# Optimization experiments

Measured on AMD Instinct MI355X. Metric: run time of the kernel, lower is better.

Reference implementation:

```python
import jax, jax.numpy as jnp
import numpy as np

D_MODEL = 512
HIDDEN_MULT = 4
D_FF = D_MODEL * HIDDEN_MULT
B, L = 4, 1024


def setup_inputs() -> dict:
    key = jax.random.key(0)
    ks = jax.random.split(key, 7)
    s1 = 1.0 / np.sqrt(D_MODEL)
    s2 = 1.0 / np.sqrt(D_FF)
    return {
        "x": jax.random.normal(ks[0], (B, L, D_MODEL), dtype=jnp.float32),
        "W1": jax.random.uniform(ks[1], (D_FF, D_MODEL), minval=-s1, maxval=s1, dtype=jnp.float32),
        "b1": jax.random.uniform(ks[2], (D_FF,), minval=-s1, maxval=s1, dtype=jnp.float32),
        "W2": jax.random.uniform(ks[3], (D_MODEL, D_FF), minval=-s2, maxval=s2, dtype=jnp.float32),
        "b2": jax.random.uniform(ks[4], (D_MODEL,), minval=-s2, maxval=s2, dtype=jnp.float32),
        "Lambda_raw_F": jax.random.uniform(ks[5], (D_FF, D_MODEL), minval=-3.0, maxval=3.0, dtype=jnp.float32),
        "Gamma_F": jax.random.uniform(ks[6], (D_FF, D_MODEL), minval=-0.5 * s1, maxval=0.5 * s1, dtype=jnp.float32),
    }


def _stp_forward(x, W1, b1, W2, b2, Lambda_raw_F, Gamma_F):
    # x: (B, L, D)
    retention = 1.0 - jax.nn.sigmoid(Lambda_raw_F)  # (d_ff, D)
    gamma = Gamma_F
    # static contribution of W1: (B, L, d_ff)
    static_h = jnp.einsum('bld,fd->blf', x, W1) + b1

    def step(F_state, inputs):
        # F_state: (B, d_ff, D); x_t: (B, D); sh_t: (B, d_ff)
        x_t, sh_t = inputs
        h_pre = sh_t + jnp.einsum('bfd,bd->bf', F_state, x_t)
        h = jax.nn.gelu(h_pre, approximate=False)
        out = jnp.einsum('bf,df->bd', h, W2) + b2
        # Hebbian outer-product update
        F_new = retention[None] * F_state + gamma[None] * (h_pre[:, :, None] * x_t[:, None, :])
        return F_new, out

    F0 = jnp.zeros((x.shape[0], W1.shape[0], W1.shape[1]), dtype=x.dtype)
    xs = (jnp.swapaxes(x, 0, 1), jnp.swapaxes(static_h, 0, 1))  # (L, B, ...)
    _, ys = jax.lax.scan(step, F0, xs)
    return jnp.swapaxes(ys, 0, 1)  # (B, L, D)


def reference(x, W1, b1, W2, b2, Lambda_raw_F, Gamma_F):
    return _stp_forward(x, W1, b1, W2, b2, Lambda_raw_F, Gamma_F)
```

## Files before the change

### kernel.cpp

```cpp
#include <hip/hip_runtime.h>
#include <cstdint>

#define DM   512
#define DFF  2048
#define BSZ  4
#define LSEQ 1024

__device__ __forceinline__ float4 f4fma(float4 a, float4 b, float4 c) {
    return make_float4(fmaf(a.x, b.x, c.x), fmaf(a.y, b.y, c.y),
                       fmaf(a.z, b.z, c.z), fmaf(a.w, b.w, c.w));
}
__device__ __forceinline__ float4 f4mul(float4 a, float4 b) {
    return make_float4(a.x * b.x, a.y * b.y, a.z * b.z, a.w * b.w);
}
__device__ __forceinline__ float4 f4fmas(float4 a, float s, float4 c) {
    return make_float4(fmaf(a.x, s, c.x), fmaf(a.y, s, c.y),
                       fmaf(a.z, s, c.z), fmaf(a.w, s, c.w));
}

__device__ __forceinline__ float red32(float p) {
    int t;
    t = __builtin_amdgcn_update_dpp(0, __float_as_int(p), 0xB1, 0xF, 0xF, true);
    p += __int_as_float(t);
    t = __builtin_amdgcn_update_dpp(0, __float_as_int(p), 0x4E, 0xF, 0xF, true);
    p += __int_as_float(t);
    p += __int_as_float(__builtin_amdgcn_ds_swizzle(__float_as_int(p), 0x101F));
    p += __int_as_float(__builtin_amdgcn_ds_swizzle(__float_as_int(p), 0x201F));
    p += __int_as_float(__builtin_amdgcn_ds_swizzle(__float_as_int(p), 0x401F));
    return p;
}

__global__ __launch_bounds__(256, 4)
void stp_scan(const float* __restrict__ x,
              const float* __restrict__ Lam,
              const float* __restrict__ Gam,
              float* __restrict__ hbuf)
{
    const int lane = threadIdx.x & 63;
    const int wid  = threadIdx.x >> 6;
    const int j    = lane & 31;
    const int h    = lane >> 5;
    const int b    = blockIdx.x >> 8;
    const int f    = ((blockIdx.x & 255) << 3) + (wid << 1) + h;

    const float4* __restrict__ x4 =
        reinterpret_cast<const float4*>(x + (size_t)b * LSEQ * DM);
    float* __restrict__ hrow = hbuf + (size_t)b * LSEQ * DFF + f;

    float4 F0 = make_float4(0.f,0.f,0.f,0.f), F1 = F0, F2 = F0, F3 = F0;
    float4 R0, R1, R2, R3, G0, G1, G2, G3;
    {
        const float4* lr = reinterpret_cast<const float4*>(Lam + (size_t)f * DM);
        const float4* gr = reinterpret_cast<const float4*>(Gam + (size_t)f * DM);
        float4 l0 = lr[j], l1 = lr[j + 32], l2 = lr[j + 64], l3 = lr[j + 96];
        #define SIGM(dst, src)                                   \
            dst.x = 1.0f / (1.0f + expf(src.x));                 \
            dst.y = 1.0f / (1.0f + expf(src.y));                 \
            dst.z = 1.0f / (1.0f + expf(src.z));                 \
            dst.w = 1.0f / (1.0f + expf(src.w));
        SIGM(R0, l0) SIGM(R1, l1) SIGM(R2, l2) SIGM(R3, l3)
        #undef SIGM
        G0 = gr[j]; G1 = gr[j + 32]; G2 = gr[j + 64]; G3 = gr[j + 96];
    }

#define STP_STEP(T, Xa, Xb, Xc, Xd, SH)                                   \
    {                                                                     \
        float4 a = f4fma(F1, (Xb), f4mul(F0, (Xa)));                      \
        float4 c = f4fma(F3, (Xd), f4mul(F2, (Xc)));                      \
        a.x += c.x; a.y += c.y; a.z += c.z; a.w += c.w;                   \
        float p = (a.x + a.y) + (a.z + a.w);                              \
        p = red32(p);                                                     \
        const float hp = p + (SH);                                        \
        if (j == 0) hrow[(size_t)(T) * DFF] = hp;                         \
        float4 t0 = f4mul(R0, F0), g0 = f4mul(G0, (Xa));                  \
        float4 t1 = f4mul(R1, F1), g1 = f4mul(G1, (Xb));                  \
        float4 t2 = f4mul(R2, F2), g2 = f4mul(G2, (Xc));                  \
        float4 t3 = f4mul(R3, F3), g3 = f4mul(G3, (Xd));                  \
        F0 = f4fmas(g0, hp, t0);                                          \
        F1 = f4fmas(g1, hp, t1);                                          \
        F2 = f4fmas(g2, hp, t2);                                          \
        F3 = f4fmas(g3, hp, t3);                                          \
    }

    float4 xA0 = x4[j], xA1 = x4[j + 32], xA2 = x4[j + 64], xA3 = x4[j + 96];
    float  shA = hrow[0];

    #pragma unroll 1
    for (int t = 0; t < LSEQ; t += 2) {
        const int o1 = (t + 1) * 128;
        float4 xB0 = x4[o1 + j],      xB1 = x4[o1 + 32 + j];
        float4 xB2 = x4[o1 + 64 + j], xB3 = x4[o1 + 96 + j];
        float  shB = hrow[(size_t)(t + 1) * DFF];

        STP_STEP(t, xA0, xA1, xA2, xA3, shA)

        const int t2 = (t + 2 < LSEQ) ? (t + 2) : (LSEQ - 1);
        const int o2 = t2 * 128;
        xA0 = x4[o2 + j];      xA1 = x4[o2 + 32 + j];
        xA2 = x4[o2 + 64 + j]; xA3 = x4[o2 + 96 + j];
        shA = hrow[(size_t)t2 * DFF];

        STP_STEP(t + 1, xB0, xB1, xB2, xB3, shB)
    }
#undef STP_STEP
}

__global__ __launch_bounds__(256)
void gelu_inplace(float4* __restrict__ p, int n4)
{
    int i = blockIdx.x * blockDim.x + threadIdx.x;
    const int stride = gridDim.x * blockDim.x;
    for (; i < n4; i += stride) {
        float4 v = p[i];
        v.x = 0.5f * v.x * (1.0f + erff(v.x * 0.70710678118654752f));
        v.y = 0.5f * v.y * (1.0f + erff(v.y * 0.70710678118654752f));
        v.z = 0.5f * v.z * (1.0f + erff(v.z * 0.70710678118654752f));
        v.w = 0.5f * v.w * (1.0f + erff(v.w * 0.70710678118654752f));
        p[i] = v;
    }
}

__global__ __launch_bounds__(256)
void gemm_nt_bias(const float* __restrict__ A,
                  const float* __restrict__ Bm,
                  const float* __restrict__ bias,
                  float* __restrict__ C,
                  int M, int N, int K)
{
    __shared__ float As[16][68];
    __shared__ float Bs[16][68];

    const int tid = threadIdx.x;
    const int tx  = tid & 15;
    const int ty  = tid >> 4;
    const int row0 = blockIdx.y * 64;
    const int col0 = blockIdx.x * 64;

    const int lr = tid >> 2;
    const int lk = (tid & 3) << 2;

    const float* Aptr = A  + (size_t)(row0 + lr) * K + lk;
    const float* Bptr = Bm + (size_t)(col0 + lr) * K + lk;

    float acc[4][4] = {};
    float4 av = *reinterpret_cast<const float4*>(Aptr);
    float4 bv = *reinterpret_cast<const float4*>(Bptr);

    const int NT = K >> 4;
    for (int kt = 0; kt < NT; ++kt) {
        __syncthreads();
        As[lk + 0][lr] = av.x; As[lk + 1][lr] = av.y;
        As[lk + 2][lr] = av.z; As[lk + 3][lr] = av.w;
        Bs[lk + 0][lr] = bv.x; Bs[lk + 1][lr] = bv.y;
        Bs[lk + 2][lr] = bv.z; Bs[lk + 3][lr] = bv.w;
        __syncthreads();

        if (kt + 1 < NT) {
            av = *reinterpret_cast<const float4*>(Aptr + (kt + 1) * 16);
            bv = *reinterpret_cast<const float4*>(Bptr + (kt + 1) * 16);
        }

        #pragma unroll
        for (int k = 0; k < 16; ++k) {
            float4 a = *reinterpret_cast<const float4*>(&As[k][ty * 4]);
            float4 bb = *reinterpret_cast<const float4*>(&Bs[k][tx * 4]);
            acc[0][0] = fmaf(a.x, bb.x, acc[0][0]);
            acc[0][1] = fmaf(a.x, bb.y, acc[0][1]);
            acc[0][2] = fmaf(a.x, bb.z, acc[0][2]);
            acc[0][3] = fmaf(a.x, bb.w, acc[0][3]);
            acc[1][0] = fmaf(a.y, bb.x, acc[1][0]);
            acc[1][1] = fmaf(a.y, bb.y, acc[1][1]);
            acc[1][2] = fmaf(a.y, bb.z, acc[1][2]);
            acc[1][3] = fmaf(a.y, bb.w, acc[1][3]);
            acc[2][0] = fmaf(a.z, bb.x, acc[2][0]);
            acc[2][1] = fmaf(a.z, bb.y, acc[2][1]);
            acc[2][2] = fmaf(a.z, bb.z, acc[2][2]);
            acc[2][3] = fmaf(a.z, bb.w, acc[2][3]);
            acc[3][0] = fmaf(a.w, bb.x, acc[3][0]);
            acc[3][1] = fmaf(a.w, bb.y, acc[3][1]);
            acc[3][2] = fmaf(a.w, bb.z, acc[3][2]);
            acc[3][3] = fmaf(a.w, bb.w, acc[3][3]);
        }
    }

    const float4 bb = *reinterpret_cast<const float4*>(&bias[col0 + tx * 4]);
    #pragma unroll
    for (int i = 0; i < 4; ++i) {
        float4 o;
        o.x = acc[i][0] + bb.x;
        o.y = acc[i][1] + bb.y;
        o.z = acc[i][2] + bb.z;
        o.w = acc[i][3] + bb.w;
        *reinterpret_cast<float4*>(&C[(size_t)(row0 + ty * 4 + i) * N + col0 + tx * 4]) = o;
    }
}

extern "C" void kernel_launch(void* const* d_in, const int* in_sizes, int n_in,
                              void* d_out, int out_size, void* d_ws, size_t ws_size,
                              hipStream_t stream)
{
    const float* x   = (const float*)d_in[0];
    const float* W1  = (const float*)d_in[1];
    const float* b1  = (const float*)d_in[2];
    const float* W2  = (const float*)d_in[3];
    const float* b2  = (const float*)d_in[4];
    const float* Lam = (const float*)d_in[5];
    const float* Gam = (const float*)d_in[6];
    float* out  = (float*)d_out;
    float* hbuf = (float*)d_ws;

    const int M = BSZ * LSEQ;

    gemm_nt_bias<<<dim3(DFF / 64, M / 64), dim3(256), 0, stream>>>(
        x, W1, b1, hbuf, M, DFF, DM);

    stp_scan<<<dim3(BSZ * (DFF / 8)), dim3(256), 0, stream>>>(x, Lam, Gam, hbuf);

    gelu_inplace<<<dim3(2048), dim3(256), 0, stream>>>(
        reinterpret_cast<float4*>(hbuf), M * DFF / 4);

    gemm_nt_bias<<<dim3(DM / 64, M / 64), dim3(256), 0, stream>>>(
        hbuf, W2, b2, out, M, DM, DFF);
}
```

Baseline: 836.4 us.

## Stage x timesteps through double-buffered LDS and use packed FP32 math

Each block now loads the x row for a timestep once into a double-buffered shared-memory tile and synchronizes between steps, instead of every wave re-reading x from global memory. The inner products and state update are rewritten with v_pk_mul/v_pk_fma packed FP32 inline asm, and the cross-lane reduction uses row_shr DPP plus a broadcast swizzle. This cuts global load traffic and VALU instruction count, but adds two __syncthreads per step pair that couple the four waves, and inline asm may limit compiler scheduling.

After: 777.9 us. 1.08x faster.

```diff
diff --git a/kernel.cpp b/kernel.cpp
--- a/kernel.cpp
+++ b/kernel.cpp
@@ -6,29 +6,27 @@
 #define BSZ  4
 #define LSEQ 1024
 
-__device__ __forceinline__ float4 f4fma(float4 a, float4 b, float4 c) {
-    return make_float4(fmaf(a.x, b.x, c.x), fmaf(a.y, b.y, c.y),
-                       fmaf(a.z, b.z, c.z), fmaf(a.w, b.w, c.w));
-}
-__device__ __forceinline__ float4 f4mul(float4 a, float4 b) {
-    return make_float4(a.x * b.x, a.y * b.y, a.z * b.z, a.w * b.w);
-}
-__device__ __forceinline__ float4 f4fmas(float4 a, float s, float4 c) {
-    return make_float4(fmaf(a.x, s, c.x), fmaf(a.y, s, c.y),
-                       fmaf(a.z, s, c.z), fmaf(a.w, s, c.w));
-}
-
-__device__ __forceinline__ float red32(float p) {
-    int t;
-    t = __builtin_amdgcn_update_dpp(0, __float_as_int(p), 0xB1, 0xF, 0xF, true);
-    p += __int_as_float(t);
-    t = __builtin_amdgcn_update_dpp(0, __float_as_int(p), 0x4E, 0xF, 0xF, true);
-    p += __int_as_float(t);
-    p += __int_as_float(__builtin_amdgcn_ds_swizzle(__float_as_int(p), 0x101F));
-    p += __int_as_float(__builtin_amdgcn_ds_swizzle(__float_as_int(p), 0x201F));
-    p += __int_as_float(__builtin_amdgcn_ds_swizzle(__float_as_int(p), 0x401F));
-    return p;
-}
+typedef __attribute__((ext_vector_type(2))) float f32x2;
+
+__device__ __forceinline__ f32x2 pk_mul(f32x2 a, f32x2 b) {
+    f32x2 d;
+    asm("v_pk_mul_f32 %0, %1, %2" : "=v"(d) : "v"(a), "v"(b));
+    return d;
+}
+__device__ __forceinline__ f32x2 pk_fma(f32x2 a, f32x2 b, f32x2 c) {
+    f32x2 d;
+    asm("v_pk_fma_f32 %0, %1, %2, %3" : "=v"(d) : "v"(a), "v"(b), "v"(c));
+    return d;
+}
+__device__ __forceinline__ f32x2 pk_add(f32x2 a, f32x2 b) {
+    f32x2 d;
+    asm("v_pk_add_f32 %0, %1, %2" : "=v"(d) : "v"(a), "v"(b));
+    return d;
+}
+
+#define DPP_ADD(p, ctrl)                                                     \
+    p += __int_as_float(__builtin_amdgcn_update_dpp(                         \
+        0, __float_as_int(p), (ctrl), 0xF, 0xF, true))
 
 __global__ __launch_bounds__(256, 4)
 void stp_scan(const float* __restrict__ x,
@@ -36,71 +34,104 @@
               const float* __restrict__ Gam,
               float* __restrict__ hbuf)
 {
-    const int lane = threadIdx.x & 63;
-    const int wid  = threadIdx.x >> 6;
+    const int tid  = threadIdx.x;
+    const int lane = tid & 63;
+    const int wid  = tid >> 6;
     const int j    = lane & 31;
     const int h    = lane >> 5;
     const int b    = blockIdx.x >> 8;
     const int f    = ((blockIdx.x & 255) << 3) + (wid << 1) + h;
 
-    const float4* __restrict__ x4 =
+    __shared__ float4 xs[2][128];
+
+    const float4* __restrict__ x4g =
         reinterpret_cast<const float4*>(x + (size_t)b * LSEQ * DM);
-    float* __restrict__ hrow = hbuf + (size_t)b * LSEQ * DFF + f;
-
-    float4 F0 = make_float4(0.f,0.f,0.f,0.f), F1 = F0, F2 = F0, F3 = F0;
-    float4 R0, R1, R2, R3, G0, G1, G2, G3;
+    float* __restrict__ hbase = hbuf + (size_t)b * LSEQ * DFF;
+
+    f32x2 F[8], R[8], G[8];
     {
         const float4* lr = reinterpret_cast<const float4*>(Lam + (size_t)f * DM);
         const float4* gr = reinterpret_cast<const float4*>(Gam + (size_t)f * DM);
-        float4 l0 = lr[j], l1 = lr[j + 32], l2 = lr[j + 64], l3 = lr[j + 96];
-        #define SIGM(dst, src)                                   \
-            dst.x = 1.0f / (1.0f + expf(src.x));                 \
-            dst.y = 1.0f / (1.0f + expf(src.y));                 \
-            dst.z = 1.0f / (1.0f + expf(src.z));                 \
-            dst.w = 1.0f / (1.0f + expf(src.w));
-        SIGM(R0, l0) SIGM(R1, l1) SIGM(R2, l2) SIGM(R3, l3)
-        #undef SIGM
-        G0 = gr[j]; G1 = gr[j + 32]; G2 = gr[j + 64]; G3 = gr[j + 96];
-    }
-
-#define STP_STEP(T, Xa, Xb, Xc, Xd, SH)                                   \
-    {                                                                     \
-        float4 a = f4fma(F1, (Xb), f4mul(F0, (Xa)));                      \
-        float4 c = f4fma(F3, (Xd), f4mul(F2, (Xc)));                      \
-        a.x += c.x; a.y += c.y; a.z += c.z; a.w += c.w;                   \
-        float p = (a.x + a.y) + (a.z + a.w);                              \
-        p = red32(p);                                                     \
-        const float hp = p + (SH);                                        \
-        if (j == 0) hrow[(size_t)(T) * DFF] = hp;                         \
-        float4 t0 = f4mul(R0, F0), g0 = f4mul(G0, (Xa));                  \
-        float4 t1 = f4mul(R1, F1), g1 = f4mul(G1, (Xb));                  \
-        float4 t2 = f4mul(R2, F2), g2 = f4mul(G2, (Xc));                  \
-        float4 t3 = f4mul(R3, F3), g3 = f4mul(G3, (Xd));                  \
-        F0 = f4fmas(g0, hp, t0);                                          \
-        F1 = f4fmas(g1, hp, t1);                                          \
-        F2 = f4fmas(g2, hp, t2);                                          \
-        F3 = f4fmas(g3, hp, t3);                                          \
-    }
-
-    float4 xA0 = x4[j], xA1 = x4[j + 32], xA2 = x4[j + 64], xA3 = x4[j + 96];
-    float  shA = hrow[0];
+        #pragma unroll
+        for (int k = 0; k < 4; ++k) {
+            float4 lv = lr[j + 32 * k];
+            float4 gv = gr[j + 32 * k];
+            f32x2 r0, r1;
+            r0.x = 1.0f / (1.0f + expf(lv.x));
+            r0.y = 1.0f / (1.0f + expf(lv.y));
+            r1.x = 1.0f / (1.0f + expf(lv.z));
+            r1.y = 1.0f / (1.0f + expf(lv.w));
+            R[2 * k] = r0;   R[2 * k + 1] = r1;
+            f32x2 g0; g0.x = gv.x; g0.y = gv.y;
+            f32x2 g1; g1.x = gv.z; g1.y = gv.w;
+            G[2 * k] = g0;   G[2 * k + 1] = g1;
+            f32x2 z; z.x = 0.f; z.y = 0.f;
+            F[2 * k] = z;    F[2 * k + 1] = z;
+        }
+    }
+
+#define STP_STEP(T, CUR, SHV)                                                 \
+    {                                                                         \
+        float4 q0 = xs[CUR][j];                                               \
+        float4 q1 = xs[CUR][j + 32];                                          \
+        float4 q2 = xs[CUR][j + 64];                                          \
+        float4 q3 = xs[CUR][j + 96];                                          \
+        f32x2 x0 = *(f32x2*)&q0.x, x1 = *(f32x2*)&q0.z;                       \
+        f32x2 x2 = *(f32x2*)&q1.x, x3 = *(f32x2*)&q1.z;                       \
+        f32x2 x4_ = *(f32x2*)&q2.x, x5 = *(f32x2*)&q2.z;                      \
+        f32x2 x6 = *(f32x2*)&q3.x, x7 = *(f32x2*)&q3.z;                       \
+        f32x2 a0 = pk_mul(F[0], x0); f32x2 a1 = pk_mul(F[2], x2);             \
+        a0 = pk_fma(F[1], x1, a0);   a1 = pk_fma(F[3], x3, a1);               \
+        a0 = pk_fma(F[4], x4_, a0);  a1 = pk_fma(F[5], x5, a1);               \
+        a0 = pk_fma(F[6], x6, a0);   a1 = pk_fma(F[7], x7, a1);               \
+        f32x2 asum = pk_add(a0, a1);                                          \
+        float p = asum.x + asum.y;                                            \
+        DPP_ADD(p, 0x111);                                    \
+        DPP_ADD(p, 0x112);                                    \
+        DPP_ADD(p, 0x114);                                    \
+        DPP_ADD(p, 0x118);                                    \
+        DPP_ADD(p, 0x142);            \
+        float hpv = __int_as_float(                                           \
+            __builtin_amdgcn_ds_swizzle(__float_as_int(p), 0x3E0)) + (SHV);   \
+        if (j == 0) hbase[(size_t)(T) * DFF + f] = hpv;                       \
+        f32x2 hp2; hp2.x = hpv; hp2.y = hpv;                                  \
+        F[0] = pk_fma(pk_mul(G[0], x0), hp2, pk_mul(R[0], F[0]));             \
+        F[1] = pk_fma(pk_mul(G[1], x1), hp2, pk_mul(R[1], F[1]));             \
+        F[2] = pk_fma(pk_mul(G[2], x2), hp2, pk_mul(R[2], F[2]));             \
+        F[3] = pk_fma(pk_mul(G[3], x3), hp2, pk_mul(R[3], F[3]));             \
+        F[4] = pk_fma(pk_mul(G[4], x4_), hp2, pk_mul(R[4], F[4]));            \
+        F[5] = pk_fma(pk_mul(G[5], x5), hp2, pk_mul(R[5], F[5]));             \
+        F[6] = pk_fma(pk_mul(G[6], x6), hp2, pk_mul(R[6], F[6]));             \
+        F[7] = pk_fma(pk_mul(G[7], x7), hp2, pk_mul(R[7], F[7]));             \
+    }
+
+    float4 stgA, stgB;
+    if (tid < 128) {
+        xs[0][tid] = x4g[tid];
+        stgA = x4g[128 + tid];
+    }
+    float shA = hbase[f];
+    float shB = hbase[(size_t)DFF + f];
+    __syncthreads();
 
     #pragma unroll 1
     for (int t = 0; t < LSEQ; t += 2) {
-        const int o1 = (t + 1) * 128;
-        float4 xB0 = x4[o1 + j],      xB1 = x4[o1 + 32 + j];
-        float4 xB2 = x4[o1 + 64 + j], xB3 = x4[o1 + 96 + j];
-        float  shB = hrow[(size_t)(t + 1) * DFF];
-
-        STP_STEP(t, xA0, xA1, xA2, xA3, shA)
-
-        const int t2 = (t + 2 < LSEQ) ? (t + 2) : (LSEQ - 1);
-        const int o2 = t2 * 128;
-        xA0 = x4[o2 + j];      xA1 = x4[o2 + 32 + j];
-        xA2 = x4[o2 + 64 + j]; xA3 = x4[o2 + 96 + j];
-        shA = hrow[(size_t)t2 * DFF];
-
-        STP_STEP(t + 1, xB0, xB1, xB2, xB3, shB)
+        STP_STEP(t, 0, shA)
+        if (tid < 128) xs[1][tid] = stgA;
+        __syncthreads();
+        {
+            const int tl = (t + 2 < LSEQ) ? t + 2 : LSEQ - 1;
+            if (tid < 128) stgB = x4g[tl * 128 + tid];
+            shA = hbase[(size_t)tl * DFF + f];
+        }
+        STP_STEP(t + 1, 1, shB)
+        if (tid < 128) xs[0][tid] = stgB;
+        __syncthreads();
+        {
+            const int tl = (t + 3 < LSEQ) ? t + 3 : LSEQ - 1;
+            if (tid < 128) stgA = x4g[tl * 128 + tid];
+            shB = hbase[(size_t)tl * DFF + f];
+        }
     }
 #undef STP_STEP
 }
```
